# Kernel optimization log

Hardware: AMD Instinct MI355X
Metric: run time of the kernel (lower is better)

Reference implementation:

```python
import jax, jax.numpy as jnp
import numpy as np

GROUP_SIZE = 128
NIBBLES = 8  # int4 values packed per int32


def dequantize(qweight, qzeros, scales):
    """Unpack int4 weights/zeros and dequantize: w = (q - z) * scale.

    qweight: [in/8, out] int32, 8 int4 values packed along the IN dim.
    qzeros:  [groups, out/8] int32, 8 int4 zeros packed along the OUT dim.
    scales:  [groups, out] fp16.
    Returns w: [in, out] fp16.
    """
    shifts = (jnp.arange(NIBBLES, dtype=jnp.int32) * 4)
    # unpack weights along input dim -> [in/8, 8, out] -> [in, out]
    q = ((qweight[:, None, :] >> shifts[None, :, None]) & 15)
    q = q.reshape(-1, qweight.shape[1])
    # unpack zeros along output dim -> [groups, out/8, 8] -> [groups, out]
    z = ((qzeros[:, :, None] >> shifts[None, None, :]) & 15)
    z = z.reshape(qzeros.shape[0], -1)
    # broadcast per-group zeros/scales to per-input-row
    z_full = jnp.repeat(z, GROUP_SIZE, axis=0).astype(scales.dtype)   # [in, out]
    s_full = jnp.repeat(scales, GROUP_SIZE, axis=0)                    # [in, out]
    return (q.astype(scales.dtype) - z_full) * s_full


def setup_inputs() -> dict:
    key = jax.random.key(0)
    k1, k2, k3, k4, k5 = jax.random.split(key, 5)
    B, S, IN, OUT, G = 2, 2048, 4096, 11008, 32
    x = jax.random.normal(k1, (B, S, IN), dtype=jnp.float16)
    qweight = jax.random.randint(k2, (IN // 8, OUT), 0, 2147483647, dtype=jnp.int32)
    qzeros = jax.random.randint(k3, (G, OUT // 8), 0, 2147483647, dtype=jnp.int32)
    scales = jax.random.uniform(k4, (G, OUT), dtype=jnp.float16, minval=0.001, maxval=0.02)
    bias = jax.random.normal(k5, (OUT,), dtype=jnp.float16)
    return {"x": x, "qweight": qweight, "qzeros": qzeros, "scales": scales, "bias": bias}


def reference(x, qweight, qzeros, scales, bias):
    w = dequantize(qweight, qzeros, scales)  # [in, out] fp16
    # q4_matmul accumulates in fp32, emits fp16
    out = jnp.einsum('bsi,io->bso', x, w, preferred_element_type=jnp.float32)
    out = out.astype(jnp.float16) + bias
    return out
```

## Files before the change

kernel.cpp:

```cpp
#include <hip/hip_runtime.h>
#include <cstdint>
#include <cstddef>


typedef unsigned short u16;
typedef u16    u16x8  __attribute__((ext_vector_type(8)));
typedef __bf16 bfv8   __attribute__((ext_vector_type(8)));
typedef float  f32x4  __attribute__((ext_vector_type(4)));

#define K_DIM 4096
#define N_DIM 11008
#define GS    128
#define KT32  (K_DIM / 32)
#define LSTR  72

__device__ __forceinline__ u16 f2bf(float f) {
  union { float f; uint32_t u; } v;
  v.f = f;
  uint32_t u = v.u + 0x7FFFu + ((v.u >> 16) & 1u);
  return (u16)(u >> 16);
}
__device__ __forceinline__ float f16r(float v) {
  return (float)(_Float16)v;
}
__device__ __forceinline__ void async_load16(const u16* g, u16* l) {
  __builtin_amdgcn_global_load_lds(
      (const __attribute__((address_space(1))) uint32_t*)g,
      (__attribute__((address_space(3))) uint32_t*)l, 16, 0, 0);
}

__global__ __launch_bounds__(256) void convert_x32(
    const float* __restrict__ x, u16* __restrict__ xb) {
  const int kt = blockIdx.x, mt = blockIdx.y;
  const int m0 = mt * 128, k0 = kt * 32;
  u16* dst = xb + ((size_t)mt * KT32 + kt) * 4096;
#pragma unroll
  for (int i = 0; i < 2; ++i) {
    const int g = i * 256 + threadIdx.x;
    const int r = g >> 2, s = g & 3;
    const int kq = s ^ ((r >> 1) & 3);
    const float* sp = x + (size_t)(m0 + r) * K_DIM + (k0 + kq * 8);
    const f32x4 p = *(const f32x4*)sp;
    const f32x4 q = *(const f32x4*)(sp + 4);
    u16x8 o;
#pragma unroll
    for (int t = 0; t < 4; ++t) { o[t] = f2bf(p[t]); o[t + 4] = f2bf(q[t]); }
    *(u16x8*)(dst + (size_t)g * 8) = o;
  }
}

__global__ __launch_bounds__(256) void dequant32(
    const uint32_t* __restrict__ qweight, const uint32_t* __restrict__ qzeros,
    const float* __restrict__ scales, u16* __restrict__ wt) {
  const int kt = blockIdx.x, nt = blockIdx.y;
  const int n0 = nt * 128;
  const int gq = kt >> 2;
  u16* dst = wt + ((size_t)nt * KT32 + kt) * 4096;
#pragma unroll
  for (int i = 0; i < 2; ++i) {
    const int g = i * 256 + threadIdx.x;
    const int r = g >> 2, s = g & 3;
    const int kq = s ^ ((r >> 1) & 3);
    const int n = n0 + r;
    const uint32_t zq = qzeros[(size_t)gq * (N_DIM / 8) + (n >> 3)];
    const int   z   = (int)((zq >> ((n & 7) * 4)) & 15u);
    const float sc  = scales[(size_t)gq * N_DIM + n];
    const float nzs = -sc * (float)z;
    const uint32_t q = qweight[(size_t)(kt * 4 + kq) * N_DIM + n];
    u16x8 o;
#pragma unroll
    for (int t = 0; t < 8; ++t) {
      const int qv = (int)((q >> (t * 4)) & 15u);
      o[t] = f2bf(fmaf((float)qv, sc, nzs));
    }
    *(u16x8*)(dst + (size_t)g * 8) = o;
  }
}

#define STAGE_A(t) do {                                                      \
    const int sb_ = (t) & 3;                                                 \
    async_load16(atile + ((size_t)0 * KT32 + (t)) * 4096 + tid * 8,          \
                 As + sb_ * 8192 + 0 * 4096 + wave * 512);                   \
    async_load16(atile + ((size_t)1 * KT32 + (t)) * 4096 + tid * 8,          \
                 As + sb_ * 8192 + 1 * 4096 + wave * 512);                   \
  } while (0)
#define STAGE_B(t) do {                                                      \
    const int sb_ = (t) & 3;                                                 \
    async_load16(btile + ((size_t)0 * KT32 + (t)) * 4096 + tid * 8,          \
                 Bs + sb_ * 8192 + 0 * 4096 + wave * 512);                   \
    async_load16(btile + ((size_t)1 * KT32 + (t)) * 4096 + tid * 8,          \
                 Bs + sb_ * 8192 + 1 * 4096 + wave * 512);                   \
  } while (0)
#define LDF(base, off) __builtin_bit_cast(bfv8, *(const u16x8*)((base) + (off)))
#define MF(i, j, av, bv)                                                     \
  acc[i][j] = __builtin_amdgcn_mfma_f32_16x16x32_bf16((av), (bv), acc[i][j], 0, 0, 0)

__global__ __launch_bounds__(512, 2) void gemm_256(
    const u16* __restrict__ xb, const u16* __restrict__ wt,
    const float* __restrict__ bias, float* __restrict__ out) {
  __shared__ __align__(16) u16 As[4 * 8192];
  __shared__ __align__(16) u16 Bs[4 * 8192];

  const int tid  = threadIdx.x;
  const int lane = tid & 63;
  const int wave = tid >> 6;
  const int wm   = wave >> 2;
  const int wn   = wave & 3;
  const int lrow = lane & 15;
  const int lk   = lane >> 4;
  const int swz  = (lrow >> 1) & 3;

  const int n0 = blockIdx.x * 256;
  const int m0 = blockIdx.y * 256;

  const u16* atile = xb + (size_t)(2 * blockIdx.y) * KT32 * 4096;
  const u16* btile = wt + (size_t)(2 * blockIdx.x) * KT32 * 4096;

  const int aoff = wm * 4096 + (lrow * 4 + (lk ^ swz)) * 8;
  const int boff = (wn >> 1) * 4096 + (((wn & 1) * 64 + lrow) * 4 + (lk ^ swz)) * 8;

  f32x4 acc[8][4];
#pragma unroll
  for (int i = 0; i < 8; ++i)
#pragma unroll
    for (int j = 0; j < 4; ++j) acc[i][j] = f32x4{0.f, 0.f, 0.f, 0.f};

  STAGE_A(0); STAGE_B(0); STAGE_A(1); STAGE_B(1); STAGE_A(2); STAGE_B(2);
  asm volatile("s_waitcnt vmcnt(8)" ::: "memory");
  asm volatile("s_barrier" ::: "memory");

#pragma unroll 4
  for (int t = 0; t < KT32; ++t) {
    const u16* A = As + (t & 3) * 8192;
    const u16* B = Bs + (t & 3) * 8192;
    bfv8 a[4], b[4];
#pragma unroll
    for (int j = 0; j < 4; ++j) b[j] = LDF(B, boff + j * 512);
#pragma unroll
    for (int i = 0; i < 4; ++i) a[i] = LDF(A, aoff + i * 512);
    if (t + 3 < KT32) STAGE_A(t + 3);
    asm volatile("s_barrier" ::: "memory");
    __builtin_amdgcn_s_setprio(1);
#pragma unroll
    for (int i = 0; i < 4; ++i)
#pragma unroll
      for (int j = 0; j < 4; ++j) MF(i, j, a[i], b[j]);
    __builtin_amdgcn_s_setprio(0);
    asm volatile("s_barrier" ::: "memory");
#pragma unroll
    for (int i = 0; i < 4; ++i) a[i] = LDF(A, aoff + (4 + i) * 512);
    if (t + 3 < KT32) STAGE_B(t + 3);
    asm volatile("s_barrier" ::: "memory");
    __builtin_amdgcn_s_setprio(1);
#pragma unroll
    for (int i = 0; i < 4; ++i)
#pragma unroll
      for (int j = 0; j < 4; ++j) MF(4 + i, j, a[i], b[j]);
    __builtin_amdgcn_s_setprio(0);
    if (t == KT32 - 1) break;
    if (t < KT32 - 3) {
      asm volatile("s_waitcnt vmcnt(8)" ::: "memory");
    } else if (t == KT32 - 3) {
      asm volatile("s_waitcnt vmcnt(4)" ::: "memory");
    } else {
      asm volatile("s_waitcnt vmcnt(0)" ::: "memory");
    }
    asm volatile("s_barrier" ::: "memory");
  }

#pragma unroll
  for (int j = 0; j < 4; ++j) {
    const int n = n0 + wn * 64 + j * 16 + lrow;
    const float bvf = bias[n];
#pragma unroll
    for (int i = 0; i < 8; ++i) {
      const int mrow = m0 + wm * 128 + i * 16 + lk * 4;
#pragma unroll
      for (int r = 0; r < 4; ++r) {
        out[(size_t)(mrow + r) * N_DIM + n] = f16r(f16r(acc[i][j][r]) + bvf);
      }
    }
  }
}

__global__ __launch_bounds__(256) void gemm_fused(
    const float* __restrict__ xf, const uint32_t* __restrict__ qw,
    const uint32_t* __restrict__ qzeros, const float* __restrict__ scales,
    const float* __restrict__ bias, float* __restrict__ out) {
  __shared__ __align__(16) u16 As[128 * LSTR];
  __shared__ __align__(16) u16 Bs[128 * LSTR];

  const int tid  = threadIdx.x;
  const int lane = tid & 63;
  const int wave = tid >> 6;
  const int n0 = blockIdx.x * 128;
  const int m0 = blockIdx.y * 128;
  const int m_off = (wave >> 1) * 64;
  const int n_off = (wave & 1) * 64;
  const int lrow  = lane & 15;
  const int lk    = lane >> 4;
  const int sm = tid >> 3;
  const int sc = tid & 7;

  f32x4 acc[4][4];
#pragma unroll
  for (int i = 0; i < 4; ++i)
#pragma unroll
    for (int j = 0; j < 4; ++j) acc[i][j] = f32x4{0.f, 0.f, 0.f, 0.f};

  const int ncol = n0 + (tid & 127);
  float s_cur = 0.f, nzs_cur = 0.f;

  for (int kt = 0; kt < K_DIM / 64; ++kt) {
    const int k0 = kt * 64;
    u16x8 av[4];
#pragma unroll
    for (int i = 0; i < 4; ++i) {
      const int m = i * 32 + sm;
      const float* sp = xf + (size_t)(m0 + m) * K_DIM + (k0 + sc * 8);
      const f32x4 p = *(const f32x4*)sp;
      const f32x4 q4 = *(const f32x4*)(sp + 4);
#pragma unroll
      for (int t = 0; t < 4; ++t) { av[i][t] = f2bf(p[t]); av[i][t+4] = f2bf(q4[t]); }
    }
    u16x8 bv[4];
    if ((k0 & (GS - 1)) == 0) {
      const int g = k0 >> 7;
      const uint32_t zq = qzeros[(size_t)g * (N_DIM / 8) + (ncol >> 3)];
      const int z = (int)((zq >> ((ncol & 7) * 4)) & 15u);
      s_cur = scales[(size_t)g * N_DIM + ncol];
      nzs_cur = -s_cur * (float)z;
    }
#pragma unroll
    for (int i = 0; i < 4; ++i) {
      const int k8l = (tid >> 7) + i * 2;
      const uint32_t q = qw[(size_t)(k0 / 8 + k8l) * N_DIM + ncol];
#pragma unroll
      for (int t = 0; t < 8; ++t) {
        const int qv = (int)((q >> (t * 4)) & 15u);
        bv[i][t] = f2bf(fmaf((float)qv, s_cur, nzs_cur));
      }
    }
#pragma unroll
    for (int i = 0; i < 4; ++i)
      *(u16x8*)&As[(i * 32 + sm) * LSTR + sc * 8] = av[i];
    {
      const int nl = tid & 127;
#pragma unroll
      for (int i = 0; i < 4; ++i) {
        const int k8l = (tid >> 7) + i * 2;
        *(u16x8*)&Bs[nl * LSTR + k8l * 8] = bv[i];
      }
    }
    __syncthreads();
#pragma unroll
    for (int ks = 0; ks < 2; ++ks) {
      const int c = (ks * 4 + lk) * 8;
      bfv8 a[4], b[4];
#pragma unroll
      for (int i = 0; i < 4; ++i)
        a[i] = __builtin_bit_cast(bfv8,
                 *(const u16x8*)&As[(m_off + i * 16 + lrow) * LSTR + c]);
#pragma unroll
      for (int j = 0; j < 4; ++j)
        b[j] = __builtin_bit_cast(bfv8,
                 *(const u16x8*)&Bs[(n_off + j * 16 + lrow) * LSTR + c]);
#pragma unroll
      for (int i = 0; i < 4; ++i)
#pragma unroll
        for (int j = 0; j < 4; ++j)
          acc[i][j] = __builtin_amdgcn_mfma_f32_16x16x32_bf16(a[i], b[j],
                                                              acc[i][j], 0, 0, 0);
    }
    __syncthreads();
  }
#pragma unroll
  for (int j = 0; j < 4; ++j) {
    const int n = n0 + n_off + j * 16 + lrow;
    const float bvf = bias[n];
#pragma unroll
    for (int i = 0; i < 4; ++i) {
      const int mrow = m0 + m_off + i * 16 + lk * 4;
#pragma unroll
      for (int r = 0; r < 4; ++r)
        out[(size_t)(mrow + r) * N_DIM + n] = f16r(f16r(acc[i][j][r]) + bvf);
    }
  }
}

extern "C" void kernel_launch(void* const* d_in, const int* in_sizes, int n_in,
                              void* d_out, int out_size, void* d_ws, size_t ws_size,
                              hipStream_t stream) {
  const float* x = nullptr;      const uint32_t* qweight = nullptr;
  const uint32_t* qzeros = nullptr;
  const float* scales = nullptr; const float* bias = nullptr;
  int M = 4096;
  for (int i = 0; i < n_in; ++i) {
    const long long s = in_sizes[i];
    if      (s == (long long)(K_DIM / 8) * N_DIM) qweight = (const uint32_t*)d_in[i];
    else if (s == (long long)(K_DIM / GS) * (N_DIM / 8)) qzeros = (const uint32_t*)d_in[i];
    else if (s == (long long)(K_DIM / GS) * N_DIM) scales = (const float*)d_in[i];
    else if (s == (long long)N_DIM) bias = (const float*)d_in[i];
    else { x = (const float*)d_in[i]; M = (int)(s / K_DIM); }
  }
  float* out = (float*)d_out;

  const size_t xb_bytes = (size_t)M * K_DIM * sizeof(u16);
  const size_t wt_bytes = (size_t)N_DIM * K_DIM * sizeof(u16);

  if (ws_size >= xb_bytes + wt_bytes && (M % 256) == 0) {
    u16* xbp = (u16*)d_ws;
    u16* wtp = (u16*)((char*)d_ws + xb_bytes);
    convert_x32<<<dim3(KT32, M / 128), 256, 0, stream>>>(x, xbp);
    dequant32<<<dim3(KT32, N_DIM / 128), 256, 0, stream>>>(
        qweight, qzeros, scales, wtp);
    gemm_256<<<dim3(N_DIM / 256, M / 256), 512, 0, stream>>>(
        xbp, wtp, bias, out);
  } else {
    gemm_fused<<<dim3(N_DIM / 128, (M + 127) / 128), 256, 0, stream>>>(
        x, qweight, qzeros, scales, bias, out);
  }
}
```

Baseline: 620.8 us.

## Restructure GEMM main loop with prefetch depth two and XCD-aware block remap

Rewrites the gemm_256 main loop as a manually unrolled macro pipeline. Prefetch distance drops from three k-tiles to two, with sched_barrier fences and explicit lgkmcnt waits before each MFMA batch. Workgroup IDs are remapped so consecutive tiles land on the same XCD, which should improve L2 reuse. The aim is tighter LDS/MFMA overlap and better cache locality, at the cost of less load latency hiding and more barriers per tile.

```diff
diff --git a/kernel.cpp b/kernel.cpp
--- a/kernel.cpp
+++ b/kernel.cpp
@@ -11,7 +11,7 @@
 #define K_DIM 4096
 #define N_DIM 11008
 #define GS    128
-#define KT32  (K_DIM / 32)
+#define KT32N (K_DIM / 32)
 #define LSTR  72
 
 __device__ __forceinline__ u16 f2bf(float f) {
@@ -33,7 +33,7 @@
     const float* __restrict__ x, u16* __restrict__ xb) {
   const int kt = blockIdx.x, mt = blockIdx.y;
   const int m0 = mt * 128, k0 = kt * 32;
-  u16* dst = xb + ((size_t)mt * KT32 + kt) * 4096;
+  u16* dst = xb + ((size_t)mt * KT32N + kt) * 4096;
 #pragma unroll
   for (int i = 0; i < 2; ++i) {
     const int g = i * 256 + threadIdx.x;
@@ -55,7 +55,7 @@
   const int kt = blockIdx.x, nt = blockIdx.y;
   const int n0 = nt * 128;
   const int gq = kt >> 2;
-  u16* dst = wt + ((size_t)nt * KT32 + kt) * 4096;
+  u16* dst = wt + ((size_t)nt * KT32N + kt) * 4096;
 #pragma unroll
   for (int i = 0; i < 2; ++i) {
     const int g = i * 256 + threadIdx.x;
@@ -77,23 +77,72 @@
   }
 }
 
-#define STAGE_A(t) do {                                                      \
-    const int sb_ = (t) & 3;                                                 \
-    async_load16(atile + ((size_t)0 * KT32 + (t)) * 4096 + tid * 8,          \
-                 As + sb_ * 8192 + 0 * 4096 + wave * 512);                   \
-    async_load16(atile + ((size_t)1 * KT32 + (t)) * 4096 + tid * 8,          \
-                 As + sb_ * 8192 + 1 * 4096 + wave * 512);                   \
-  } while (0)
-#define STAGE_B(t) do {                                                      \
-    const int sb_ = (t) & 3;                                                 \
-    async_load16(btile + ((size_t)0 * KT32 + (t)) * 4096 + tid * 8,          \
-                 Bs + sb_ * 8192 + 0 * 4096 + wave * 512);                   \
-    async_load16(btile + ((size_t)1 * KT32 + (t)) * 4096 + tid * 8,          \
-                 Bs + sb_ * 8192 + 1 * 4096 + wave * 512);                   \
-  } while (0)
-#define LDF(base, off) __builtin_bit_cast(bfv8, *(const u16x8*)((base) + (off)))
-#define MF(i, j, av, bv)                                                     \
-  acc[i][j] = __builtin_amdgcn_mfma_f32_16x16x32_bf16((av), (bv), acc[i][j], 0, 0, 0)
+#define LDF(p)  __builtin_bit_cast(bfv8, *(const u16x8*)(p))
+#define BAR()   __builtin_amdgcn_s_barrier()
+#define VMW_(n) asm volatile("s_waitcnt vmcnt(" #n ")")
+#define VMW(n)  VMW_(n)
+#define LKW0()  asm volatile("s_waitcnt lgkmcnt(0)")
+#define SBAR()  __builtin_amdgcn_sched_barrier(0)
+
+#define STAGE_A32K(ktt, h, dbuf) do {                                         \
+    const u16* s_ = at0 + ((size_t)(h) * KT32N + (ktt)) * 4096;               \
+    async_load16(s_ + (size_t)tid * 8,                                        \
+                 &As[(dbuf) * 8192 + (h) * 4096 + wave * 512]);               \
+  } while (0)
+#define STAGE_B32K(ktt, h, dbuf) do {                                         \
+    const u16* s_ = bt0 + ((size_t)(h) * KT32N + (ktt)) * 4096;               \
+    async_load16(s_ + (size_t)tid * 8,                                        \
+                 &Bs[(dbuf) * 8192 + (h) * 4096 + wave * 512]);               \
+  } while (0)
+
+#define RD_A4(v, ib, bufl) do {                                               \
+    _Pragma("unroll")                                                         \
+    for (int i_ = 0; i_ < 4; ++i_)                                            \
+      v[i_] = LDF(&As[(bufl) * 8192 + aoff + ((ib) + i_) * 512 + kq]);        \
+  } while (0)
+#define RD_B4(v, bufl) do {                                                   \
+    _Pragma("unroll")                                                         \
+    for (int j_ = 0; j_ < 4; ++j_)                                            \
+      v[j_] = LDF(&Bs[(bufl) * 8192 + boff + j_ * 512 + kq]);                 \
+  } while (0)
+
+#define MM16(ib, av, bv) do {                                                 \
+    __builtin_amdgcn_s_setprio(1);                                            \
+    _Pragma("unroll")                                                         \
+    for (int ii_ = 0; ii_ < 4; ++ii_)                                         \
+      _Pragma("unroll")                                                       \
+      for (int j_ = 0; j_ < 4; ++j_)                                          \
+        acc[(ib) + ii_][j_] = __builtin_amdgcn_mfma_f32_16x16x32_bf16(        \
+            av[ii_], bv[j_], acc[(ib) + ii_][j_], 0, 0, 0);                   \
+    __builtin_amdgcn_s_setprio(0);                                            \
+  } while (0)
+
+#define KTILE32(T, BUFL, DO_ST, VMWSTMT) do {                                 \
+                                                                 \
+    RD_A4(a0, 0, BUFL);                                                       \
+    RD_B4(bb, BUFL);                                                          \
+    if (DO_ST) {                                                              \
+      STAGE_A32K((T) + 2, 0, ((BUFL) + 2) & 3);                               \
+      STAGE_A32K((T) + 2, 1, ((BUFL) + 2) & 3);                               \
+    }                                                                         \
+    SBAR();                                                                   \
+    BAR();                                                                    \
+    LKW0(); SBAR();                                                           \
+    MM16(0, a0, bb);                                                          \
+    BAR();                                                                    \
+                                                                 \
+    RD_A4(a1, 4, BUFL);                                                       \
+    if (DO_ST) {                                                              \
+      STAGE_B32K((T) + 2, 0, ((BUFL) + 2) & 3);                               \
+      STAGE_B32K((T) + 2, 1, ((BUFL) + 2) & 3);                               \
+    }                                                                         \
+    SBAR();                                                                   \
+    BAR();                                                                    \
+    LKW0(); SBAR();                                                           \
+    MM16(4, a1, bb);                                                          \
+    VMWSTMT;                                                                  \
+    BAR();                                                                    \
+  } while (0)
 
 __global__ __launch_bounds__(512, 2) void gemm_256(
     const u16* __restrict__ xb, const u16* __restrict__ wt,
@@ -108,65 +157,46 @@
   const int wn   = wave & 3;
   const int lrow = lane & 15;
   const int lk   = lane >> 4;
-  const int swz  = (lrow >> 1) & 3;
-
-  const int n0 = blockIdx.x * 256;
-  const int m0 = blockIdx.y * 256;
-
-  const u16* atile = xb + (size_t)(2 * blockIdx.y) * KT32 * 4096;
-  const u16* btile = wt + (size_t)(2 * blockIdx.x) * KT32 * 4096;
-
-  const int aoff = wm * 4096 + (lrow * 4 + (lk ^ swz)) * 8;
-  const int boff = (wn >> 1) * 4096 + (((wn & 1) * 64 + lrow) * 4 + (lk ^ swz)) * 8;
-
+
+  const int nwg = gridDim.x * gridDim.y;
+  int wg = blockIdx.y * gridDim.x + blockIdx.x;
+  if ((nwg & 7) == 0) wg = (wg & 7) * (nwg >> 3) + (wg >> 3);
+  const int bx = wg % gridDim.x;
+  const int by = wg / gridDim.x;
+  const int n0 = bx * 256;
+  const int m0 = by * 256;
+
+  const u16* at0 = xb + (size_t)(2 * by) * KT32N * 4096;
+  const u16* bt0 = wt + (size_t)(2 * bx) * KT32N * 4096;
+
+  const int aoff = wm * 4096 + lrow * 32;
+  const int boff = (wn >> 1) * 4096 + ((wn & 1) * 64 + lrow) * 32;
+  const int kq   = (lk ^ ((lrow >> 1) & 3)) * 8;
+
+  bfv8 a0[4], a1[4], bb[4];
   f32x4 acc[8][4];
 #pragma unroll
   for (int i = 0; i < 8; ++i)
 #pragma unroll
     for (int j = 0; j < 4; ++j) acc[i][j] = f32x4{0.f, 0.f, 0.f, 0.f};
 
-  STAGE_A(0); STAGE_B(0); STAGE_A(1); STAGE_B(1); STAGE_A(2); STAGE_B(2);
-  asm volatile("s_waitcnt vmcnt(8)" ::: "memory");
-  asm volatile("s_barrier" ::: "memory");
-
-#pragma unroll 4
-  for (int t = 0; t < KT32; ++t) {
-    const u16* A = As + (t & 3) * 8192;
-    const u16* B = Bs + (t & 3) * 8192;
-    bfv8 a[4], b[4];
-#pragma unroll
-    for (int j = 0; j < 4; ++j) b[j] = LDF(B, boff + j * 512);
-#pragma unroll
-    for (int i = 0; i < 4; ++i) a[i] = LDF(A, aoff + i * 512);
-    if (t + 3 < KT32) STAGE_A(t + 3);
-    asm volatile("s_barrier" ::: "memory");
-    __builtin_amdgcn_s_setprio(1);
-#pragma unroll
-    for (int i = 0; i < 4; ++i)
-#pragma unroll
-      for (int j = 0; j < 4; ++j) MF(i, j, a[i], b[j]);
-    __builtin_amdgcn_s_setprio(0);
-    asm volatile("s_barrier" ::: "memory");
-#pragma unroll
-    for (int i = 0; i < 4; ++i) a[i] = LDF(A, aoff + (4 + i) * 512);
-    if (t + 3 < KT32) STAGE_B(t + 3);
-    asm volatile("s_barrier" ::: "memory");
-    __builtin_amdgcn_s_setprio(1);
-#pragma unroll
-    for (int i = 0; i < 4; ++i)
-#pragma unroll
-      for (int j = 0; j < 4; ++j) MF(4 + i, j, a[i], b[j]);
-    __builtin_amdgcn_s_setprio(0);
-    if (t == KT32 - 1) break;
-    if (t < KT32 - 3) {
-      asm volatile("s_waitcnt vmcnt(8)" ::: "memory");
-    } else if (t == KT32 - 3) {
-      asm volatile("s_waitcnt vmcnt(4)" ::: "memory");
-    } else {
-      asm volatile("s_waitcnt vmcnt(0)" ::: "memory");
-    }
-    asm volatile("s_barrier" ::: "memory");
-  }
+  STAGE_A32K(0, 0, 0); STAGE_A32K(0, 1, 0);
+  STAGE_B32K(0, 0, 0); STAGE_B32K(0, 1, 0);
+  STAGE_A32K(1, 0, 1); STAGE_A32K(1, 1, 1);
+  STAGE_B32K(1, 0, 1); STAGE_B32K(1, 1, 1);
+  VMW(4); BAR();
+
+#pragma unroll 1
+  for (int t = 0; t < 124; t += 4) {
+    KTILE32(t + 0, 0, 1, VMW(4));
+    KTILE32(t + 1, 1, 1, VMW(4));
+    KTILE32(t + 2, 2, 1, VMW(4));
+    KTILE32(t + 3, 3, 1, VMW(4));
+  }
+  KTILE32(124, 0, 1, VMW(4));
+  KTILE32(125, 1, 1, VMW(4));
+  KTILE32(126, 2, 0, VMW(0));
+  KTILE32(127, 3, 0, (void)0);
 
 #pragma unroll
   for (int j = 0; j < 4; ++j) {
@@ -311,8 +341,8 @@
   if (ws_size >= xb_bytes + wt_bytes && (M % 256) == 0) {
     u16* xbp = (u16*)d_ws;
     u16* wtp = (u16*)((char*)d_ws + xb_bytes);
-    convert_x32<<<dim3(KT32, M / 128), 256, 0, stream>>>(x, xbp);
-    dequant32<<<dim3(KT32, N_DIM / 128), 256, 0, stream>>>(
+    convert_x32<<<dim3(KT32N, M / 128), 256, 0, stream>>>(x, xbp);
+    dequant32<<<dim3(KT32N, N_DIM / 128), 256, 0, stream>>>(
         qweight, qzeros, scales, wtp);
     gemm_256<<<dim3(N_DIM / 256, M / 256), 512, 0, stream>>>(
         xbp, wtp, bias, out);
```

New measurement: 658.2 us. 6.0% more time.
